# Optimization experiments

Hardware: AMD Instinct MI355X
Metric: run time of the kernel (lower is better)

## Reference

```python
import jax, jax.numpy as jnp
import numpy as np

N, D, G, C, M = 4096, 256, 4, 10, 5  # nodes, feat dim, batches, centroids, clusterings


def setup_inputs() -> dict:
    key = jax.random.key(0)
    k1, k2, k3, k4 = jax.random.split(key, 4)
    adj = jax.random.uniform(k1, (N, N), dtype=jnp.float32)
    enc_rep = jax.random.normal(k2, (N, D), dtype=jnp.float32)
    batch_id = jax.random.randint(k3, (N,), 0, G, dtype=jnp.int32)
    cluster_labels = jax.random.randint(k4, (M, N), 0, C, dtype=jnp.int32)
    return {"adj": adj, "enc_rep": enc_rep, "batch_id": batch_id,
            "cluster_labels": cluster_labels, "top_k": 20, "top_k_inter": 10}


def reference(adj, enc_rep, batch_id, cluster_labels, top_k, top_k_inter):
    n = enc_rep.shape[0]
    NEG = jnp.float32(-1e30)
    rows = jnp.arange(n)

    # 'similarity' metric: raw inner-product similarity, full N x N once
    sim = enc_rep @ enc_rep.T                                # [N, N]
    same = batch_id[:, None] == batch_id[None, :]            # same-batch mask

    # intra: top_k+1 within own batch group, drop first (self) column
    intra_sim = jnp.where(same, sim, NEG)
    _, intra_idx = jax.lax.top_k(intra_sim, top_k + 1)
    intra_idx = intra_idx[:, 1:]                              # [N, top_k]

    # inter: top_k_inter among all other batch groups
    inter_sim = jnp.where(same, NEG, sim)
    _, inter_idx = jax.lax.top_k(inter_sim, top_k_inter)      # [N, top_k_inter]

    knn_idx = jnp.concatenate([intra_idx, inter_idx], axis=1)  # [N, k_tot]

    # rep_adj[j, i] = 1 iff j is a knn of i  (coo rows=neighbors, cols=node)
    B = jnp.zeros((n, n), jnp.float32).at[knn_idx, rows[:, None]].set(1.0)
    # common_adj = rep_adj * (rep_adj.T > 0), diag zeroed (mutual-knn graph)
    common = B * B.T
    common = common.at[rows, rows].set(0.0)

    # locality = knn_neighbor * adj
    locality = common * adj

    # padded-neighbor validity mask (I_knn_padded != -1 analog): mutual neighbors
    mutual = common[rows[:, None], knn_idx] > 0               # [N, k_tot]

    # per-clustering close-neighbor test, combined across clusterings
    nb_lbl = cluster_labels[:, knn_idx]                       # [M, N, k_tot]
    eq = cluster_labels[:, :, None] == nb_lbl                 # [M, N, k_tot]
    curr = eq | mutual[None]                                  # curr_close_nei = eq | bool_mask
    all_close = jnp.all(curr, axis=0)                         # AND across clusterings

    return locality, all_close.astype(jnp.float32)
```

## Files before the change

kernel.cpp:

```cpp
#include <hip/hip_runtime.h>
#include <hip/hip_bf16.h>
#include <cfloat>

#define NN 4096
#define DD 256
#define MM 5
#define GG 4
#define K_TOT 30
#define TGT_INTRA 32
#define TGT_INTER 24
#define CAND_CAP 64

typedef __attribute__((ext_vector_type(8))) short bf16x8;
typedef __attribute__((ext_vector_type(4))) float f32x4;

__device__ __forceinline__ void async16(const void* g, void* l) {
    __builtin_amdgcn_global_load_lds((__attribute__((address_space(1))) void*)g,
                                     (__attribute__((address_space(3))) void*)l,
                                     16, 0, 0);
}

__global__ __launch_bounds__(256) void convert_bf16(const float* __restrict__ E,
                                                    ushort* __restrict__ Eb) {
    const int idx = blockIdx.x * 256 + threadIdx.x;
    const float4 f = ((const float4*)E)[idx];
    ushort4 h;
    {
        __hip_bfloat16 a = __float2bfloat16(f.x); h.x = *(ushort*)&a;
        __hip_bfloat16 b = __float2bfloat16(f.y); h.y = *(ushort*)&b;
        __hip_bfloat16 c = __float2bfloat16(f.z); h.z = *(ushort*)&c;
        __hip_bfloat16 d = __float2bfloat16(f.w); h.w = *(ushort*)&d;
    }
    ((ushort4*)Eb)[idx] = h;
}

__global__ __launch_bounds__(256) void build_mask(const int* __restrict__ batch,
                                                  unsigned long long* __restrict__ maskTab) {
    const int j = blockIdx.x * 256 + threadIdx.x;
    const int b = batch[j];
    const int wv = j >> 6;
#pragma unroll
    for (int g = 0; g < GG; ++g) {
        const unsigned long long m = __ballot(b != g);
        if ((threadIdx.x & 63) == 0) maskTab[g * (NN / 64) + wv] = m;
    }
}

__global__ __launch_bounds__(256) void gemm_bf16(const ushort* __restrict__ Eb,
                                                 ushort* __restrict__ simb) {
    __shared__ union {
        struct { ushort A[128 * 32]; ushort B[128 * 32]; } s;
        ushort stage[32 * 136];
    } lds;

    const int t = threadIdx.x;
    const int w = t >> 6, lane = t & 63;
    const int quad = lane >> 4, mr = lane & 15;
    const int rowBase = blockIdx.y * 128, colBase = blockIdx.x * 128;
    const int waveRow = (w & 1) * 64, waveCol = (w >> 1) * 64;

    const int lrow = lane >> 2;
    const int lslot = lane & 3;
    const int gchunk = lslot ^ ((lrow >> 1) & 3);

    f32x4 acc[4][4];
#pragma unroll
    for (int a = 0; a < 4; ++a)
#pragma unroll
        for (int b = 0; b < 4; ++b) acc[a][b] = (f32x4)(0.0f);

    for (int kc = 0; kc < DD; kc += 32) {
#pragma unroll
        for (int n = 0; n < 2; ++n) {
            const int r = w * 32 + n * 16 + lrow;
            const ushort* ga = Eb + (size_t)(rowBase + r) * DD + kc + gchunk * 8;
            const ushort* gb = Eb + (size_t)(colBase + r) * DD + kc + gchunk * 8;
            async16(ga, &lds.s.A[(w * 32 + n * 16) * 32]);
            async16(gb, &lds.s.B[(w * 32 + n * 16) * 32]);
        }
        __syncthreads();

        const int swzF = (mr >> 1) & 3;
        bf16x8 af[4], bfr[4];
#pragma unroll
        for (int rt = 0; rt < 4; ++rt)
            af[rt] = *(const bf16x8*)&lds.s.A[(waveRow + rt * 16 + mr) * 32 +
                                              ((quad ^ swzF) * 8)];
#pragma unroll
        for (int ct = 0; ct < 4; ++ct)
            bfr[ct] = *(const bf16x8*)&lds.s.B[(waveCol + ct * 16 + mr) * 32 +
                                               ((quad ^ swzF) * 8)];
#pragma unroll
        for (int rt = 0; rt < 4; ++rt)
#pragma unroll
            for (int ct = 0; ct < 4; ++ct)
                acc[rt][ct] = __builtin_amdgcn_mfma_f32_16x16x32_bf16(
                    af[rt], bfr[ct], acc[rt][ct], 0, 0, 0);
        __syncthreads();
    }

#pragma unroll
    for (int c = 0; c < 4; ++c) {
        __syncthreads();
        if ((w & 1) == (c >> 1)) {
            const int rtBase = 2 * (c & 1);
#pragma unroll
            for (int r2 = 0; r2 < 2; ++r2) {
                const int rt = rtBase + r2;
#pragma unroll
                for (int ct = 0; ct < 4; ++ct)
#pragma unroll
                    for (int reg = 0; reg < 4; ++reg) {
                        __hip_bfloat16 hb = __float2bfloat16(acc[rt][ct][reg]);
                        const int lr2 = r2 * 16 + quad * 4 + reg;
                        lds.stage[lr2 * 136 + waveCol + ct * 16 + mr] = *(ushort*)&hb;
                    }
            }
        }
        __syncthreads();
#pragma unroll
        for (int it = 0; it < 2; ++it) {
            const int cid = t + it * 256;
            const int row = cid >> 4;
            const int off = (cid & 15) * 8;
            *(int4*)(simb + (size_t)(rowBase + c * 32 + row) * NN + colBase + off) =
                *(const int4*)&lds.stage[row * 136 + off];
        }
    }
}

__global__ __launch_bounds__(128, 8) void select_rescore(
        const ushort* __restrict__ sim,
        const float* __restrict__ E,
        const int* __restrict__ batch,
        const unsigned long long* __restrict__ maskTab,
        int* __restrict__ knn) {
    __shared__ unsigned histS[256];
    __shared__ unsigned subS[256];
    __shared__ int candIdxS[2][CAND_CAP];
    __shared__ double candValS[2][CAND_CAP];
    __shared__ int cntS[2];
    __shared__ int cbS[2];
    __shared__ unsigned remS[2];
    __shared__ unsigned thrS[2];

    const int t = threadIdx.x;
    const int w = t >> 6, lane = t & 63;
    const int i = blockIdx.x;
    const int bi = batch[i];

    histS[t] = 0u; histS[t + 128] = 0u;
    subS[t] = 0u;  subS[t + 128] = 0u;
    if (t < 2) cntS[t] = 0;
    __syncthreads();

    unsigned kp[16];
    unsigned interm = 0;
    {
        const ushort* sp = sim + (size_t)i * NN + t * 8;
        const unsigned long long* mp = maskTab + bi * (NN / 64) + (t >> 3);
        const int sh = (t & 7) * 8;
#pragma unroll
        for (int c = 0; c < 4; ++c) {
            const int4 sv = *(const int4*)(sp + c * 1024);
            const unsigned mb = (unsigned)(mp[c * 16] >> sh) & 0xFFu;
            interm |= mb << (c * 8);
            const unsigned uu[4] = {(unsigned)sv.x, (unsigned)sv.y,
                                    (unsigned)sv.z, (unsigned)sv.w};
#pragma unroll
            for (int p = 0; p < 4; ++p) {
                const unsigned u = uu[p];
                const unsigned sgn = u & 0x80008000u;
                const unsigned k2 = u ^ (0x80008000u | ((sgn >> 15) * 0x7FFFu));
                kp[c * 4 + p] = k2;
                const unsigned m0 = (mb >> (2 * p)) & 1u;
                const unsigned m1 = (mb >> (2 * p + 1)) & 1u;
                atomicAdd(&histS[(k2 >> 8) & 0xFF], m0 ? 0x10000u : 1u);
                atomicAdd(&histS[k2 >> 24], m1 ? 0x10000u : 1u);
            }
        }
    }
    __syncthreads();

    {
        const unsigned* hb = &histS[lane * 4];
        const unsigned s4 = hb[0] + hb[1] + hb[2] + hb[3];
        unsigned suf = s4;
#pragma unroll
        for (int off = 1; off < 64; off <<= 1) {
            const unsigned o = __shfl_down(suf, off);
            if (lane + off < 64) suf += o;
        }
        unsigned cum = suf - s4;
#pragma unroll
        for (int b = 3; b >= 0; --b) {
            const unsigned h = hb[b];
            const unsigned prev = cum;
            cum += h;
            if ((cum & 0xFFFFu) >= TGT_INTRA && (prev & 0xFFFFu) < TGT_INTRA) {
                cbS[0] = lane * 4 + b;
                remS[0] = TGT_INTRA - (prev & 0xFFFFu);
            }
            if ((cum >> 16) >= TGT_INTER && (prev >> 16) < TGT_INTER) {
                cbS[1] = lane * 4 + b;
                remS[1] = TGT_INTER - (prev >> 16);
            }
        }
    }
    __syncthreads();

    {
        const int cb0 = cbS[0], cb1 = cbS[1];
#pragma unroll
        for (int c = 0; c < 4; ++c)
#pragma unroll
            for (int p = 0; p < 4; ++p) {
                const unsigned k2 = kp[c * 4 + p];
                const unsigned k0 = k2 & 0xFFFFu, k1 = k2 >> 16;
                const int m0 = (interm >> (c * 8 + 2 * p)) & 1;
                const int m1 = (interm >> (c * 8 + 2 * p + 1)) & 1;
                if ((int)(k0 >> 8) == (m0 ? cb1 : cb0))
                    atomicAdd(&subS[k0 & 0xFF], m0 ? 0x10000u : 1u);
                if ((int)(k1 >> 8) == (m1 ? cb1 : cb0))
                    atomicAdd(&subS[k1 & 0xFF], m1 ? 0x10000u : 1u);
            }
    }
    __syncthreads();

    {
        const unsigned rI = remS[0], rT = remS[1];
        const int cb0 = cbS[0], cb1 = cbS[1];
        const unsigned* sb = &subS[lane * 4];
        const unsigned s4 = sb[0] + sb[1] + sb[2] + sb[3];
        unsigned suf = s4;
#pragma unroll
        for (int off = 1; off < 64; off <<= 1) {
            const unsigned o = __shfl_down(suf, off);
            if (lane + off < 64) suf += o;
        }
        unsigned cum = suf - s4;
#pragma unroll
        for (int b = 3; b >= 0; --b) {
            const unsigned h = sb[b];
            const unsigned prev = cum;
            cum += h;
            if ((cum & 0xFFFFu) >= rI && (prev & 0xFFFFu) < rI)
                thrS[0] = ((unsigned)cb0 << 8) | (unsigned)(lane * 4 + b);
            if ((cum >> 16) >= rT && (prev >> 16) < rT)
                thrS[1] = ((unsigned)cb1 << 8) | (unsigned)(lane * 4 + b);
        }
    }
    __syncthreads();

    {
        const unsigned thr0 = thrS[0], thr1 = thrS[1];
#pragma unroll
        for (int c = 0; c < 4; ++c)
#pragma unroll
            for (int p = 0; p < 4; ++p) {
                const unsigned k2 = kp[c * 4 + p];
                const unsigned k0 = k2 & 0xFFFFu, k1 = k2 >> 16;
                const int m0 = (interm >> (c * 8 + 2 * p)) & 1;
                const int m1 = (interm >> (c * 8 + 2 * p + 1)) & 1;
                if (k0 >= (m0 ? thr1 : thr0)) {
                    const int pos = atomicAdd(&cntS[m0], 1);
                    if (pos < CAND_CAP) candIdxS[m0][pos] = c * 1024 + t * 8 + 2 * p;
                }
                if (k1 >= (m1 ? thr1 : thr0)) {
                    const int pos = atomicAdd(&cntS[m1], 1);
                    if (pos < CAND_CAP) candIdxS[m1][pos] = c * 1024 + t * 8 + 2 * p + 1;
                }
            }
    }
    __syncthreads();

    const int c0 = min(cntS[0], CAND_CAP);
    const int c1 = min(cntS[1], CAND_CAP);
    {
        const int tot = c0 + c1;
        const float* ei = E + (size_t)i * DD;
        if (t < tot) {
            const int m = (t < c0) ? 0 : 1;
            const int s = m ? (t - c0) : t;
            const int j = candIdxS[m][s];
            const float* ej = E + (size_t)j * DD;
            double a0 = 0, a1 = 0, a2 = 0, a3 = 0;
#pragma unroll 8
            for (int k = 0; k < DD; k += 4) {
                const float4 e = *(const float4*)(ej + k);
                a0 = fma((double)ei[k + 0], (double)e.x, a0);
                a1 = fma((double)ei[k + 1], (double)e.y, a1);
                a2 = fma((double)ei[k + 2], (double)e.z, a2);
                a3 = fma((double)ei[k + 3], (double)e.w, a3);
            }
            candValS[m][s] = (a0 + a1) + (a2 + a3);
        }
    }
    __syncthreads();

    if (w == 0) {
        if (lane < c0) {
            const double v = candValS[0][lane];
            const int idx = candIdxS[0][lane];
            int r = 0;
            for (int s = 0; s < c0; ++s) {
                const double o = candValS[0][s];
                const int oi = candIdxS[0][s];
                r += (o > v) || (o == v && oi < idx);
            }
            if (r >= 1 && r <= 20) knn[i * K_TOT + r - 1] = idx;
        }
    } else {
        if (lane < c1) {
            const double v = candValS[1][lane];
            const int idx = candIdxS[1][lane];
            int r = 0;
            for (int s = 0; s < c1; ++s) {
                const double o = candValS[1][s];
                const int oi = candIdxS[1][s];
                r += (o > v) || (o == v && oi < idx);
            }
            if (r < 10) knn[i * K_TOT + 20 + r] = idx;
        }
    }
}

__global__ __launch_bounds__(256) void finalize_k(const int* __restrict__ knn,
                                                  const float* __restrict__ adj,
                                                  const int* __restrict__ cl,
                                                  float* __restrict__ out) {
    const int gid = blockIdx.x * 256 + threadIdx.x;
    if (gid >= NN * K_TOT) return;
    const int i = gid / K_TOT;
    const int j = knn[gid];

    bool mutual = false;
#pragma unroll
    for (int s = 0; s < K_TOT; ++s) mutual |= (knn[j * K_TOT + s] == i);

    if (mutual) out[(size_t)i * NN + j] = adj[(size_t)i * NN + j];

    bool ac = mutual;
    if (!ac) {
        bool alleq = true;
#pragma unroll
        for (int m = 0; m < MM; ++m) alleq &= (cl[m * NN + i] == cl[m * NN + j]);
        ac = alleq;
    }
    out[(size_t)NN * NN + gid] = ac ? 1.0f : 0.0f;
}

extern "C" void kernel_launch(void* const* d_in, const int* in_sizes, int n_in,
                              void* d_out, int out_size, void* d_ws, size_t ws_size,
                              hipStream_t stream) {
    const float* adj = (const float*)d_in[0];
    const float* enc = (const float*)d_in[1];
    const int* batch = (const int*)d_in[2];
    const int* cl = (const int*)d_in[3];
    float* out = (float*)d_out;

    const size_t simB = (size_t)NN * NN * sizeof(ushort);
    const size_t ebB = (size_t)NN * DD * sizeof(ushort);
    const size_t knnB = (size_t)NN * K_TOT * sizeof(int);
    const size_t maskB = (size_t)GG * (NN / 64) * sizeof(unsigned long long);

    const dim3 gGrid(NN / 128, NN / 128);

    if (ws_size >= simB + ebB + knnB + maskB) {
        ushort* simb = (ushort*)d_ws;
        ushort* Eb = (ushort*)((char*)d_ws + simB);
        int* knn = (int*)((char*)d_ws + simB + ebB);
        unsigned long long* maskTab =
            (unsigned long long*)((char*)d_ws + simB + ebB + knnB);
        hipMemsetAsync(d_out, 0, (size_t)NN * NN * sizeof(float), stream);
        convert_bf16<<<NN * DD / 4 / 256, 256, 0, stream>>>(enc, Eb);
        build_mask<<<NN / 256, 256, 0, stream>>>(batch, maskTab);
        gemm_bf16<<<gGrid, 256, 0, stream>>>(Eb, simb);
        select_rescore<<<NN, 128, 0, stream>>>(simb, enc, batch, maskTab, knn);
        finalize_k<<<(NN * K_TOT + 255) / 256, 256, 0, stream>>>(knn, adj, cl, out);
    } else {
        ushort* simb = (ushort*)d_out;
        ushort* Eb = (ushort*)d_ws;
        int* knn = (int*)((char*)d_ws + ebB);
        unsigned long long* maskTab =
            (unsigned long long*)((char*)d_ws + ebB + knnB);
        convert_bf16<<<NN * DD / 4 / 256, 256, 0, stream>>>(enc, Eb);
        build_mask<<<NN / 256, 256, 0, stream>>>(batch, maskTab);
        gemm_bf16<<<gGrid, 256, 0, stream>>>(Eb, simb);
        select_rescore<<<NN, 128, 0, stream>>>(simb, enc, batch, maskTab, knn);
        hipMemsetAsync(d_out, 0, (size_t)NN * NN * sizeof(float), stream);
        finalize_k<<<(NN * K_TOT + 255) / 256, 256, 0, stream>>>(knn, adj, cl, out);
    }
}
```

Baseline: 203.6 us.

## Use knn bitset for mutual check and replicate LDS histogram bins

```diff
diff --git a/kernel.cpp b/kernel.cpp
--- a/kernel.cpp
+++ b/kernel.cpp
@@ -134,8 +134,10 @@
         const float* __restrict__ E,
         const int* __restrict__ batch,
         const unsigned long long* __restrict__ maskTab,
-        int* __restrict__ knn) {
-    __shared__ unsigned histS[256];
+        int* __restrict__ knn,
+        unsigned* __restrict__ bits) {
+    __shared__ unsigned histS[1024];
+    __shared__ unsigned mergedS[256];
     __shared__ unsigned subS[256];
     __shared__ int candIdxS[2][CAND_CAP];
     __shared__ double candValS[2][CAND_CAP];
@@ -146,11 +148,13 @@
 
     const int t = threadIdx.x;
     const int w = t >> 6, lane = t & 63;
+    const int rep = lane & 3;
     const int i = blockIdx.x;
     const int bi = batch[i];
 
-    histS[t] = 0u; histS[t + 128] = 0u;
-    subS[t] = 0u;  subS[t + 128] = 0u;
+#pragma unroll
+    for (int z = 0; z < 8; ++z) histS[t + z * 128] = 0u;
+    subS[t] = 0u; subS[t + 128] = 0u;
     if (t < 2) cntS[t] = 0;
     __syncthreads();
 
@@ -175,15 +179,25 @@
                 kp[c * 4 + p] = k2;
                 const unsigned m0 = (mb >> (2 * p)) & 1u;
                 const unsigned m1 = (mb >> (2 * p + 1)) & 1u;
-                atomicAdd(&histS[(k2 >> 8) & 0xFF], m0 ? 0x10000u : 1u);
-                atomicAdd(&histS[k2 >> 24], m1 ? 0x10000u : 1u);
-            }
-        }
-    }
-    __syncthreads();
-
-    {
-        const unsigned* hb = &histS[lane * 4];
+                atomicAdd(&histS[(((k2 >> 8) & 0xFF) << 2) + rep], m0 ? 0x10000u : 1u);
+                atomicAdd(&histS[((k2 >> 24) << 2) + rep], m1 ? 0x10000u : 1u);
+            }
+        }
+    }
+    __syncthreads();
+
+#pragma unroll
+    for (int k = 0; k < 8; ++k) {
+        const int wd = t + 128 * k;
+        unsigned v = histS[wd];
+        v += __shfl_xor(v, 1);
+        v += __shfl_xor(v, 2);
+        if ((lane & 3) == 0) mergedS[wd >> 2] = v;
+    }
+    __syncthreads();
+
+    {
+        const unsigned* hb = &mergedS[lane * 4];
         const unsigned s4 = hb[0] + hb[1] + hb[2] + hb[3];
         unsigned suf = s4;
 #pragma unroll
@@ -308,7 +322,10 @@
                 const int oi = candIdxS[0][s];
                 r += (o > v) || (o == v && oi < idx);
             }
-            if (r >= 1 && r <= 20) knn[i * K_TOT + r - 1] = idx;
+            if (r >= 1 && r <= 20) {
+                knn[i * K_TOT + r - 1] = idx;
+                atomicOr(&bits[((size_t)i << 7) + (idx >> 5)], 1u << (idx & 31));
+            }
         }
     } else {
         if (lane < c1) {
@@ -320,12 +337,16 @@
                 const int oi = candIdxS[1][s];
                 r += (o > v) || (o == v && oi < idx);
             }
-            if (r < 10) knn[i * K_TOT + 20 + r] = idx;
+            if (r < 10) {
+                knn[i * K_TOT + 20 + r] = idx;
+                atomicOr(&bits[((size_t)i << 7) + (idx >> 5)], 1u << (idx & 31));
+            }
         }
     }
 }
 
 __global__ __launch_bounds__(256) void finalize_k(const int* __restrict__ knn,
+                                                  const unsigned* __restrict__ bits,
                                                   const float* __restrict__ adj,
                                                   const int* __restrict__ cl,
                                                   float* __restrict__ out) {
@@ -334,9 +355,7 @@
     const int i = gid / K_TOT;
     const int j = knn[gid];
 
-    bool mutual = false;
-#pragma unroll
-    for (int s = 0; s < K_TOT; ++s) mutual |= (knn[j * K_TOT + s] == i);
+    const bool mutual = (bits[((size_t)j << 7) + (i >> 5)] >> (i & 31)) & 1u;
 
     if (mutual) out[(size_t)i * NN + j] = adj[(size_t)i * NN + j];
 
@@ -363,32 +382,37 @@
     const size_t ebB = (size_t)NN * DD * sizeof(ushort);
     const size_t knnB = (size_t)NN * K_TOT * sizeof(int);
     const size_t maskB = (size_t)GG * (NN / 64) * sizeof(unsigned long long);
+    const size_t bitsB = (size_t)NN * (NN / 8);
 
     const dim3 gGrid(NN / 128, NN / 128);
 
-    if (ws_size >= simB + ebB + knnB + maskB) {
+    if (ws_size >= simB + ebB + knnB + maskB + bitsB) {
         ushort* simb = (ushort*)d_ws;
         ushort* Eb = (ushort*)((char*)d_ws + simB);
         int* knn = (int*)((char*)d_ws + simB + ebB);
         unsigned long long* maskTab =
             (unsigned long long*)((char*)d_ws + simB + ebB + knnB);
+        unsigned* bits = (unsigned*)((char*)d_ws + simB + ebB + knnB + maskB);
         hipMemsetAsync(d_out, 0, (size_t)NN * NN * sizeof(float), stream);
+        hipMemsetAsync(bits, 0, bitsB, stream);
         convert_bf16<<<NN * DD / 4 / 256, 256, 0, stream>>>(enc, Eb);
         build_mask<<<NN / 256, 256, 0, stream>>>(batch, maskTab);
         gemm_bf16<<<gGrid, 256, 0, stream>>>(Eb, simb);
-        select_rescore<<<NN, 128, 0, stream>>>(simb, enc, batch, maskTab, knn);
-        finalize_k<<<(NN * K_TOT + 255) / 256, 256, 0, stream>>>(knn, adj, cl, out);
+        select_rescore<<<NN, 128, 0, stream>>>(simb, enc, batch, maskTab, knn, bits);
+        finalize_k<<<(NN * K_TOT + 255) / 256, 256, 0, stream>>>(knn, bits, adj, cl, out);
     } else {
         ushort* simb = (ushort*)d_out;
         ushort* Eb = (ushort*)d_ws;
         int* knn = (int*)((char*)d_ws + ebB);
         unsigned long long* maskTab =
             (unsigned long long*)((char*)d_ws + ebB + knnB);
+        unsigned* bits = (unsigned*)((char*)d_ws + ebB + knnB + maskB);
         convert_bf16<<<NN * DD / 4 / 256, 256, 0, stream>>>(enc, Eb);
         build_mask<<<NN / 256, 256, 0, stream>>>(batch, maskTab);
+        hipMemsetAsync(bits, 0, bitsB, stream);
         gemm_bf16<<<gGrid, 256, 0, stream>>>(Eb, simb);
-        select_rescore<<<NN, 128, 0, stream>>>(simb, enc, batch, maskTab, knn);
+        select_rescore<<<NN, 128, 0, stream>>>(simb, enc, batch, maskTab, knn, bits);
         hipMemsetAsync(d_out, 0, (size_t)NN * NN * sizeof(float), stream);
-        finalize_k<<<(NN * K_TOT + 255) / 256, 256, 0, stream>>>(knn, adj, cl, out);
-    }
-}
+        finalize_k<<<(NN * K_TOT + 255) / 256, 256, 0, stream>>>(knn, bits, adj, cl, out);
+    }
+}
```

Result: no change. 201.7 us (-1.0%).

## Fuse convert/mask kernels, replicate LDS histogram, replace memset with custom clear kernel

Applied to the files above, without the earlier changes.

```diff
diff --git a/kernel.cpp b/kernel.cpp
--- a/kernel.cpp
+++ b/kernel.cpp
@@ -20,9 +20,11 @@
                                      16, 0, 0);
 }
 
-__global__ __launch_bounds__(256) void convert_bf16(const float* __restrict__ E,
-                                                    ushort* __restrict__ Eb) {
-    const int idx = blockIdx.x * 256 + threadIdx.x;
+__global__ __launch_bounds__(256) void convert_and_mask(
+        const float* __restrict__ E, ushort* __restrict__ Eb,
+        const int* __restrict__ batch, unsigned long long* __restrict__ maskTab) {
+    const int t = threadIdx.x;
+    const int idx = blockIdx.x * 256 + t;
     const float4 f = ((const float4*)E)[idx];
     ushort4 h;
     {
@@ -32,17 +34,30 @@
         __hip_bfloat16 d = __float2bfloat16(f.w); h.w = *(ushort*)&d;
     }
     ((ushort4*)Eb)[idx] = h;
-}
-
-__global__ __launch_bounds__(256) void build_mask(const int* __restrict__ batch,
-                                                  unsigned long long* __restrict__ maskTab) {
-    const int j = blockIdx.x * 256 + threadIdx.x;
-    const int b = batch[j];
-    const int wv = j >> 6;
-#pragma unroll
-    for (int g = 0; g < GG; ++g) {
-        const unsigned long long m = __ballot(b != g);
-        if ((threadIdx.x & 63) == 0) maskTab[g * (NN / 64) + wv] = m;
+
+    if (blockIdx.x == 0) {
+#pragma unroll
+        for (int wv = 0; wv < NN / 256; ++wv) {
+            const int j = wv * 256 + t;
+            const int b = batch[j];
+#pragma unroll
+            for (int g = 0; g < GG; ++g) {
+                const unsigned long long m = __ballot(b != g);
+                if ((t & 63) == 0)
+                    maskTab[g * (NN / 64) + wv * 4 + (t >> 6)] = m;
+            }
+        }
+    }
+}
+
+__global__ __launch_bounds__(256) void clear_out(float4* __restrict__ p) {
+    const f32x4 z = (f32x4)(0.0f);
+    int idx = blockIdx.x * 256 + threadIdx.x;
+    const int stride = gridDim.x * 256;
+#pragma unroll
+    for (int r = 0; r < 8; ++r) {
+        *(f32x4*)&p[idx] = z;
+        idx += stride;
     }
 }
 
@@ -135,7 +150,8 @@
         const int* __restrict__ batch,
         const unsigned long long* __restrict__ maskTab,
         int* __restrict__ knn) {
-    __shared__ unsigned histS[256];
+    __shared__ unsigned histS[1024];
+    __shared__ unsigned mergedS[256];
     __shared__ unsigned subS[256];
     __shared__ int candIdxS[2][CAND_CAP];
     __shared__ double candValS[2][CAND_CAP];
@@ -146,11 +162,13 @@
 
     const int t = threadIdx.x;
     const int w = t >> 6, lane = t & 63;
+    const int rep = lane & 3;
     const int i = blockIdx.x;
     const int bi = batch[i];
 
-    histS[t] = 0u; histS[t + 128] = 0u;
-    subS[t] = 0u;  subS[t + 128] = 0u;
+#pragma unroll
+    for (int z = 0; z < 8; ++z) histS[t + z * 128] = 0u;
+    subS[t] = 0u; subS[t + 128] = 0u;
     if (t < 2) cntS[t] = 0;
     __syncthreads();
 
@@ -175,15 +193,25 @@
                 kp[c * 4 + p] = k2;
                 const unsigned m0 = (mb >> (2 * p)) & 1u;
                 const unsigned m1 = (mb >> (2 * p + 1)) & 1u;
-                atomicAdd(&histS[(k2 >> 8) & 0xFF], m0 ? 0x10000u : 1u);
-                atomicAdd(&histS[k2 >> 24], m1 ? 0x10000u : 1u);
-            }
-        }
-    }
-    __syncthreads();
-
-    {
-        const unsigned* hb = &histS[lane * 4];
+                atomicAdd(&histS[(((k2 >> 8) & 0xFF) << 2) + rep], m0 ? 0x10000u : 1u);
+                atomicAdd(&histS[((k2 >> 24) << 2) + rep], m1 ? 0x10000u : 1u);
+            }
+        }
+    }
+    __syncthreads();
+
+#pragma unroll
+    for (int k = 0; k < 8; ++k) {
+        const int wd = t + 128 * k;
+        unsigned v = histS[wd];
+        v += __shfl_xor(v, 1);
+        v += __shfl_xor(v, 2);
+        if ((lane & 3) == 0) mergedS[wd >> 2] = v;
+    }
+    __syncthreads();
+
+    {
+        const unsigned* hb = &mergedS[lane * 4];
         const unsigned s4 = hb[0] + hb[1] + hb[2] + hb[3];
         unsigned suf = s4;
 #pragma unroll
@@ -372,11 +400,10 @@
         int* knn = (int*)((char*)d_ws + simB + ebB);
         unsigned long long* maskTab =
             (unsigned long long*)((char*)d_ws + simB + ebB + knnB);
-        hipMemsetAsync(d_out, 0, (size_t)NN * NN * sizeof(float), stream);
-        convert_bf16<<<NN * DD / 4 / 256, 256, 0, stream>>>(enc, Eb);
-        build_mask<<<NN / 256, 256, 0, stream>>>(batch, maskTab);
+        convert_and_mask<<<NN * DD / 4 / 256, 256, 0, stream>>>(enc, Eb, batch, maskTab);
         gemm_bf16<<<gGrid, 256, 0, stream>>>(Eb, simb);
         select_rescore<<<NN, 128, 0, stream>>>(simb, enc, batch, maskTab, knn);
+        clear_out<<<2048, 256, 0, stream>>>((float4*)out);
         finalize_k<<<(NN * K_TOT + 255) / 256, 256, 0, stream>>>(knn, adj, cl, out);
     } else {
         ushort* simb = (ushort*)d_out;
@@ -384,11 +411,10 @@
         int* knn = (int*)((char*)d_ws + ebB);
         unsigned long long* maskTab =
             (unsigned long long*)((char*)d_ws + ebB + knnB);
-        convert_bf16<<<NN * DD / 4 / 256, 256, 0, stream>>>(enc, Eb);
-        build_mask<<<NN / 256, 256, 0, stream>>>(batch, maskTab);
+        convert_and_mask<<<NN * DD / 4 / 256, 256, 0, stream>>>(enc, Eb, batch, maskTab);
         gemm_bf16<<<gGrid, 256, 0, stream>>>(Eb, simb);
         select_rescore<<<NN, 128, 0, stream>>>(simb, enc, batch, maskTab, knn);
-        hipMemsetAsync(d_out, 0, (size_t)NN * NN * sizeof(float), stream);
+        clear_out<<<2048, 256, 0, stream>>>((float4*)out);
         finalize_k<<<(NN * K_TOT + 255) / 256, 256, 0, stream>>>(knn, adj, cl, out);
     }
 }
```

Result: no change. 203.3 us (-0.2%).
